# Performance work log

Measured on AMD Instinct MI355X. Metric: run time of the kernel, lower is better.

Reference implementation:

```python
import jax, jax.numpy as jnp
import numpy as np

N, D_IN, HID, NH = 16384, 2048, 2048, 16
HD = HID // NH  # head_size = 128


def setup_inputs() -> dict:
    key = jax.random.key(0)
    ks = jax.random.split(key, 8)
    s = 1.0 / np.sqrt(D_IN)
    return {
        "protein": jax.random.normal(ks[0], (N, D_IN), jnp.float32),
        "drug": jax.random.normal(ks[1], (N, D_IN), jnp.float32),
        "mask_prot": jnp.ones((N,), bool),
        "mask_drug": jnp.ones((N,), bool),
        "Wq_p": jax.random.uniform(ks[2], (D_IN, HID), jnp.float32, -s, s),
        "Wk_p": jax.random.uniform(ks[3], (D_IN, HID), jnp.float32, -s, s),
        "Wv_p": jax.random.uniform(ks[4], (D_IN, HID), jnp.float32, -s, s),
        "Wq_d": jax.random.uniform(ks[5], (D_IN, HID), jnp.float32, -s, s),
        "Wk_d": jax.random.uniform(ks[6], (D_IN, HID), jnp.float32, -s, s),
        "Wv_d": jax.random.uniform(ks[7], (D_IN, HID), jnp.float32, -s, s),
    }


def _heads(x):
    # [N, L, HID] -> [N, L, NH, HD]
    return x.reshape(x.shape[0], x.shape[1], NH, HD)


def _alpha_logits(logits, mask_row, mask_col, inf=1e6):
    # logits: [N, L1, L2, H]; masks: [N, L1], [N, L2] (broadcast over heads)
    mask_pair = mask_row[:, :, None, None] & mask_col[:, None, :, None]
    logits = jnp.where(mask_pair, logits, logits - inf)
    alpha = jax.nn.softmax(logits, axis=2)
    alpha = jnp.where(mask_row[:, :, None, None], alpha, jnp.zeros_like(alpha))
    return alpha


def reference(protein, drug, mask_prot, mask_drug, Wq_p, Wk_p, Wv_p, Wq_d, Wk_d, Wv_d):
    p = protein[:, None, :]  # [N, 1, D_IN]
    d = drug[:, None, :]
    # forward() overwrites the masks with all-ones of shape [N, L=1]
    m_p = jnp.ones(p.shape[:-1], bool)
    m_d = jnp.ones(d.shape[:-1], bool)

    qp = _heads(jnp.einsum('bld,dh->blh', p, Wq_p))  # [N,1,NH,HD]
    kp = _heads(jnp.einsum('bld,dh->blh', p, Wk_p))
    vp = _heads(jnp.einsum('bld,dh->blh', p, Wv_p))
    qd = _heads(jnp.einsum('bld,dh->blh', d, Wq_d))
    kd = _heads(jnp.einsum('bld,dh->blh', d, Wk_d))
    vd = _heads(jnp.einsum('bld,dh->blh', d, Wv_d))

    logits_pp = jnp.einsum('blhd,bkhd->blkh', qp, kp)
    logits_pd = jnp.einsum('blhd,bkhd->blkh', qp, kd)
    logits_dp = jnp.einsum('blhd,bkhd->blkh', qd, kp)
    logits_dd = jnp.einsum('blhd,bkhd->blkh', qd, kd)

    a_pp = _alpha_logits(logits_pp, m_p, m_p)
    a_pd = _alpha_logits(logits_pd, m_p, m_d)
    a_dp = _alpha_logits(logits_dp, m_d, m_p)
    a_dd = _alpha_logits(logits_dd, m_d, m_d)

    def agg(alpha, v):
        out = jnp.einsum('blkh,bkhd->blhd', alpha, v)
        return out.reshape(out.shape[0], out.shape[1], HID)

    prot_embedding = (agg(a_pp, vp) + agg(a_pd, vd)) / 2  # [N,1,HID]
    drug_embedding = (agg(a_dp, vp) + agg(a_dd, vd)) / 2

    # agg_mode == 'cls'
    prot_embed = prot_embedding[:, 0]
    drug_embed = drug_embedding[:, 0]
    return jnp.concatenate([prot_embed, drug_embed], axis=1)  # [N, 2*HID]
```

## Files before the change

### kernel.cpp

```cpp
#include <hip/hip_runtime.h>
#include <stdint.h>


typedef __attribute__((ext_vector_type(8))) short short8;
typedef __attribute__((ext_vector_type(4))) float float4v;
typedef __attribute__((ext_vector_type(2))) unsigned int uint2v;

typedef const __attribute__((address_space(1))) unsigned int* gp_t;
typedef __attribute__((address_space(3))) unsigned int* lp_t;

#define M_DIM 16384
#define N_DIM 2048
#define K_DIM 4096
#define OUT_LD 4096

static __device__ __forceinline__ unsigned int pack_bf16x2(float x, float y) {
  union { float f; unsigned int u; } a, b;
  a.f = x; b.f = y;
  unsigned int ua = a.u + 0x8000u;
  unsigned int ub = b.u + 0x8000u;
  return __builtin_amdgcn_perm(ub, ua, 0x07060302u);
}

static __device__ __forceinline__ unsigned short f2bf(float x) {
  union { float f; unsigned int u; } a; a.f = x;
  return (unsigned short)((a.u + 0x8000u) >> 16);
}

__global__ __launch_bounds__(256)
void prep_wt(const float* __restrict__ Wp, const float* __restrict__ Wd,
             unsigned short* __restrict__ Wt) {
  __shared__ float tile[32][33];
  const int k0 = blockIdx.x * 32;
  const int n0 = blockIdx.y * 32;
  const int tx = threadIdx.x;
  const int ty = threadIdx.y;
  const float* W = (k0 < 2048) ? Wp : Wd;
  const int kk0 = (k0 < 2048) ? k0 : k0 - 2048;
#pragma unroll
  for (int i = 0; i < 4; ++i) {
    int r = ty * 4 + i;
    tile[r][tx] = W[(size_t)(kk0 + r) * 2048 + n0 + tx];
  }
  __syncthreads();
#pragma unroll
  for (int i = 0; i < 4; ++i) {
    int r = ty * 4 + i;
    Wt[(size_t)(n0 + r) * (size_t)K_DIM + k0 + tx] = f2bf(tile[tx][r]);
  }
}

__global__ __launch_bounds__(256)
void cast_a(const float* __restrict__ P, const float* __restrict__ Dg,
            unsigned int* __restrict__ Abf) {
  int idx = blockIdx.x * 256 + threadIdx.x;
  int row = idx >> 10;
  int j = (idx & 1023) << 2;
  const float* src = (j < 2048) ? (P + (size_t)row * 2048 + j)
                                : (Dg + (size_t)row * 2048 + (j - 2048));
  float4v v = *(const float4v*)src;
  uint2v o;
  o.x = pack_bf16x2(v.x, v.y);
  o.y = pack_bf16x2(v.z, v.w);
  *(uint2v*)(Abf + (size_t)row * 2048 + (j >> 1)) = o;
}


#define VMW(N) asm volatile("s_waitcnt vmcnt(" #N ")" ::: "memory")
#define LGW0() asm volatile("s_waitcnt lgkmcnt(0)" ::: "memory")
#define BAR() __builtin_amdgcn_s_barrier()
#define SP1 __builtin_amdgcn_s_setprio(1);
#define SP0 __builtin_amdgcn_s_setprio(0);

__global__ __launch_bounds__(512, 1)
void gemm8(const unsigned short* __restrict__ Abf,
           const unsigned short* __restrict__ Wt,
           float* __restrict__ out) {
  __shared__ unsigned short As[2][256 * 64];
  __shared__ unsigned short Bs[2][256 * 64];

  const int t = threadIdx.x;
  const int w = t >> 6, l = t & 63;
  const int wm = w >> 2, wn = w & 3;
  const int lr = l & 15, q16 = l >> 4, xr = lr & 7;

  const int bx = blockIdx.x;
  const int logical = (bx & 7) * 64 + (bx >> 3);
  const int tn = logical & 7, tm = logical >> 3;
  const int m0 = tm << 8, n0 = tn << 8;

  const int srow = t >> 3;
  const int sk = (((t & 7) ^ (srow & 7)) << 3);
  const int brr = srow & 31;
  const int bsel = t >> 8;

  auto stage_a = [&](int buf, int k0, int h) {
#pragma unroll
    for (int sub = 0; sub < 2; ++sub) {
      const int row = m0 + sub * 128 + h * 64 + srow;
      const unsigned short* g = Abf + (size_t)row * K_DIM + (k0 + sk);
      const int ldsrow0 = sub * 128 + h * 64 + (w << 3);
      __builtin_amdgcn_global_load_lds((gp_t)(const void*)g,
                                       (lp_t)&As[buf][ldsrow0 * 64], 16, 0, 0);
    }
  };
  auto stage_b = [&](int buf, int k0, int nh) {
#pragma unroll
    for (int sub = 0; sub < 2; ++sub) {
      const int wnr = sub * 2 + bsel;
      const int ncol = n0 + wnr * 64 + nh * 32 + brr;
      const unsigned short* g = Wt + (size_t)ncol * K_DIM + (k0 + sk);
      const int ldsrow0 = wnr * 64 + nh * 32 + ((w & 3) << 3);
      __builtin_amdgcn_global_load_lds((gp_t)(const void*)g,
                                       (lp_t)&Bs[buf][ldsrow0 * 64], 16, 0, 0);
    }
  };

  float4v acc[8][4];
#pragma unroll
  for (int i = 0; i < 8; ++i)
#pragma unroll
    for (int j = 0; j < 4; ++j)
      acc[i][j] = (float4v){0.f, 0.f, 0.f, 0.f};

  const int aoff = (wm * 128 + lr) * 64;
  const int boff = (wn * 64 + lr) * 64;
  const int c0 = (q16 ^ xr) << 3;
  const int c1 = ((4 + q16) ^ xr) << 3;

  short8 aR[8][2];
  short8 bR[4][2];

  stage_a(0, 0, 0);
  stage_a(0, 0, 1);
  stage_b(0, 0, 0);
  stage_b(0, 0, 1);
  stage_a(1, 64, 0);
  stage_b(1, 64, 0);
  stage_b(1, 64, 1);
  stage_a(1, 64, 1);
  VMW(8);
  BAR();
  {
    const unsigned short* Ac = &As[0][0];
    const unsigned short* Bc = &Bs[0][0];
#pragma unroll
    for (int i = 0; i < 8; ++i) {
      aR[i][0] = *(const short8*)&Ac[aoff + i * 1024 + c0];
      aR[i][1] = *(const short8*)&Ac[aoff + i * 1024 + c1];
    }
#pragma unroll
    for (int j = 0; j < 4; ++j) {
      bR[j][0] = *(const short8*)&Bc[boff + j * 1024 + c0];
      bR[j][1] = *(const short8*)&Bc[boff + j * 1024 + c1];
    }
  }
  LGW0();
  BAR();

  auto tile_mfma = [&](const unsigned short* AcN, const unsigned short* BcN,
                       bool doread) {
    SP1
#pragma unroll
    for (int ks = 0; ks < 2; ++ks) {
      const int cks = ks ? c1 : c0;
#pragma unroll
      for (int i = 0; i < 8; ++i) {
#pragma unroll
        for (int j = 0; j < 4; ++j)
          acc[i][j] = __builtin_amdgcn_mfma_f32_16x16x32_bf16(
              aR[i][ks], bR[j][ks], acc[i][j], 0, 0, 0);
        if (doread)
          aR[i][ks] = *(const short8*)&AcN[aoff + i * 1024 + cks];
      }
      if (doread) {
#pragma unroll
        for (int j = 0; j < 4; ++j)
          bR[j][ks] = *(const short8*)&BcN[boff + j * 1024 + cks];
      }
    }
    SP0
  };

  for (int tt = 0; tt < 62; ++tt) {
    const int buf = tt & 1;
    const int k2 = tt * 64 + 128;
    stage_a(buf, k2, 0);
    stage_a(buf, k2, 1);
    stage_b(buf, k2, 0);
    stage_b(buf, k2, 1);
    tile_mfma(&As[buf ^ 1][0], &Bs[buf ^ 1][0], true);
    VMW(0);
    LGW0();
    BAR();
  }

  tile_mfma(&As[1][0], &Bs[1][0], true);
  tile_mfma(nullptr, nullptr, false);

  const int rbase = m0 + wm * 128 + q16 * 4;
  const int cbase = n0 + wn * 64 + lr;
#pragma unroll
  for (int f = 0; f < 8; ++f)
#pragma unroll
    for (int j = 0; j < 4; ++j) {
      const int row = rbase + f * 16;
      const int col = cbase + j * 16;
#pragma unroll
      for (int r = 0; r < 4; ++r) {
        float v = acc[f][j][r] * 0.5f;
        size_t o = (size_t)(row + r) * (size_t)OUT_LD + col;
        out[o] = v;
        out[o + N_DIM] = v;
      }
    }
}

__global__ __launch_bounds__(256)
void gemm_k(const float* __restrict__ Ap, const float* __restrict__ Ad,
            const unsigned short* __restrict__ Wt,
            float* __restrict__ out) {
  __shared__ unsigned short As[128 * 64];
  __shared__ unsigned short Bsm[128 * 64];

  const int t = threadIdx.x;
  const int bx = blockIdx.x;
  const int tn = bx & 15, tm = bx >> 4;
  const int m0 = tm << 7, n0 = tn << 7;
  const int w = t >> 6, l = t & 63;
  const int wmm = w & 1, wnn = w >> 1;
  const int lr = l & 15, q = l >> 4;

  const int rB = t >> 3;
  const int kB = (t & 7) * 8;

  float4v acc[4][4];
#pragma unroll
  for (int i = 0; i < 4; ++i)
#pragma unroll
    for (int j = 0; j < 4; ++j)
      acc[i][j] = (float4v){0.f, 0.f, 0.f, 0.f};

  for (int k0 = 0; k0 < K_DIM; k0 += 64) {
#pragma unroll
    for (int i = 0; i < 4; ++i) {
      const unsigned short* g =
          Wt + (size_t)(n0 + i * 32 + rB) * (size_t)K_DIM + (k0 + kB);
      __builtin_amdgcn_global_load_lds((gp_t)(const void*)g,
                                       (lp_t)&Bsm[i * 2048 + w * 512], 16, 0, 0);
    }
    {
      const float* base;
      int kk;
      if (k0 < 2048) { base = Ap; kk = k0; } else { base = Ad; kk = k0 - 2048; }
      const int rA = t >> 4;
      const int cA = (t & 15) * 4;
#pragma unroll
      for (int i = 0; i < 8; ++i) {
        int m = i * 16 + rA;
        float4v v = *(const float4v*)(base + (size_t)(m0 + m) * 2048 + kk + cA);
        uint2v o;
        o.x = pack_bf16x2(v.x, v.y);
        o.y = pack_bf16x2(v.z, v.w);
        *(uint2v*)&As[m * 64 + cA] = o;
      }
    }
    __syncthreads();

#pragma unroll
    for (int ks = 0; ks < 2; ++ks) {
      short8 a2[4], b2[4];
#pragma unroll
      for (int i = 0; i < 4; ++i) {
        a2[i] = *(const short8*)&As[(wmm * 64 + i * 16 + lr) * 64 + ks * 32 + q * 8];
        b2[i] = *(const short8*)&Bsm[(wnn * 64 + i * 16 + lr) * 64 + ks * 32 + q * 8];
      }
#pragma unroll
      for (int i = 0; i < 4; ++i)
#pragma unroll
        for (int j = 0; j < 4; ++j)
          acc[i][j] = __builtin_amdgcn_mfma_f32_16x16x32_bf16(a2[i], b2[j],
                                                              acc[i][j], 0, 0, 0);
    }
    __syncthreads();
  }

#pragma unroll
  for (int i = 0; i < 4; ++i) {
    const int r0 = m0 + wmm * 64 + i * 16 + q * 4;
#pragma unroll
    for (int j = 0; j < 4; ++j) {
      const int c = n0 + wnn * 64 + j * 16 + lr;
#pragma unroll
      for (int r = 0; r < 4; ++r) {
        float v = acc[i][j][r] * 0.5f;
        size_t o = (size_t)(r0 + r) * (size_t)OUT_LD + c;
        out[o] = v;
        out[o + 2048] = v;
      }
    }
  }
}

__global__ __launch_bounds__(256)
void gemm_fallback(const float* __restrict__ P, const float* __restrict__ Dg,
                   const float* __restrict__ Wp, const float* __restrict__ Wd,
                   float* __restrict__ out) {
  __shared__ float Asf[64][17];
  __shared__ float Bsf[16][65];
  const int bx = blockIdx.x;
  const int by = blockIdx.y;
  const int t = threadIdx.x;
  const int tc = t & 15, trw = t >> 4;
  const int m0 = by * 64, n0 = bx * 64;
  float accf[4][4] = {};
  for (int k0 = 0; k0 < 4096; k0 += 16) {
    const float* Asrc = (k0 < 2048) ? P : Dg;
    const float* Bsrc = (k0 < 2048) ? Wp : Wd;
    const int kk = k0 & 2047;
#pragma unroll
    for (int i = 0; i < 4; ++i) {
      int r = i * 16 + trw;
      Asf[r][tc] = Asrc[(size_t)(m0 + r) * 2048 + kk + tc];
    }
#pragma unroll
    for (int i = 0; i < 4; ++i) {
      int r = i * 4 + (t >> 6);
      int c = t & 63;
      Bsf[r][c] = Bsrc[(size_t)(kk + r) * 2048 + n0 + c];
    }
    __syncthreads();
#pragma unroll
    for (int k2 = 0; k2 < 16; ++k2) {
      float a[4], b[4];
#pragma unroll
      for (int i = 0; i < 4; ++i) a[i] = Asf[trw * 4 + i][k2];
#pragma unroll
      for (int j = 0; j < 4; ++j) b[j] = Bsf[k2][tc * 4 + j];
#pragma unroll
      for (int i = 0; i < 4; ++i)
#pragma unroll
        for (int j = 0; j < 4; ++j) accf[i][j] += a[i] * b[j];
    }
    __syncthreads();
  }
#pragma unroll
  for (int i = 0; i < 4; ++i)
#pragma unroll
    for (int j = 0; j < 4; ++j) {
      float v = accf[i][j] * 0.5f;
      size_t o = (size_t)(m0 + trw * 4 + i) * 4096 + n0 + tc * 4 + j;
      out[o] = v;
      out[o + 2048] = v;
    }
}

extern "C" void kernel_launch(void* const* d_in, const int* in_sizes, int n_in,
                              void* d_out, int out_size, void* d_ws, size_t ws_size,
                              hipStream_t stream) {
  const float* protein = (const float*)d_in[0];
  const float* drug    = (const float*)d_in[1];
  const float* Wv_p    = (const float*)d_in[6];
  const float* Wv_d    = (const float*)d_in[9];
  float* out = (float*)d_out;

  const size_t wt_bytes = (size_t)N_DIM * K_DIM * sizeof(unsigned short);
  const size_t a_bytes  = (size_t)M_DIM * K_DIM * sizeof(unsigned short);

  if (ws_size >= wt_bytes) {
    unsigned short* Wt = (unsigned short*)d_ws;
    prep_wt<<<dim3(128, 64), dim3(32, 8), 0, stream>>>(Wv_p, Wv_d, Wt);
    if (ws_size >= wt_bytes + a_bytes) {
      unsigned int* Abf = (unsigned int*)((char*)d_ws + wt_bytes);
      cast_a<<<65536, 256, 0, stream>>>(protein, drug, Abf);
      gemm8<<<512, 512, 0, stream>>>((const unsigned short*)Abf, Wt, out);
    } else {
      gemm_k<<<2048, 256, 0, stream>>>(protein, drug, Wt, out);
    }
  } else {
    gemm_fallback<<<dim3(32, 256), 256, 0, stream>>>(protein, drug, Wv_p, Wv_d, out);
  }
}
```

Measured before the change: 754.6 us.

## Load GEMM B operand directly from global into registers, bypassing LDS

The weight (B) tile is no longer staged through shared memory with async global-to-LDS copies. Each wave now reads its B fragments straight from global memory into registers, one k-tile ahead. The wait before the barrier is relaxed so that only the A staging loads must finish. This halves LDS footprint and LDS read traffic, but it duplicates B global reads across waves that share a column block. It also exposes global load latency with only one tile of MFMA work to hide it.

```diff
diff --git a/kernel.cpp b/kernel.cpp
--- a/kernel.cpp
+++ b/kernel.cpp
@@ -65,7 +65,6 @@
   *(uint2v*)(Abf + (size_t)row * 2048 + (j >> 1)) = o;
 }
 
-
 #define VMW(N) asm volatile("s_waitcnt vmcnt(" #N ")" ::: "memory")
 #define LGW0() asm volatile("s_waitcnt lgkmcnt(0)" ::: "memory")
 #define BAR() __builtin_amdgcn_s_barrier()
@@ -77,7 +76,6 @@
            const unsigned short* __restrict__ Wt,
            float* __restrict__ out) {
   __shared__ unsigned short As[2][256 * 64];
-  __shared__ unsigned short Bs[2][256 * 64];
 
   const int t = threadIdx.x;
   const int w = t >> 6, l = t & 63;
@@ -91,8 +89,6 @@
 
   const int srow = t >> 3;
   const int sk = (((t & 7) ^ (srow & 7)) << 3);
-  const int brr = srow & 31;
-  const int bsel = t >> 8;
 
   auto stage_a = [&](int buf, int k0, int h) {
 #pragma unroll
@@ -104,17 +100,6 @@
                                        (lp_t)&As[buf][ldsrow0 * 64], 16, 0, 0);
     }
   };
-  auto stage_b = [&](int buf, int k0, int nh) {
-#pragma unroll
-    for (int sub = 0; sub < 2; ++sub) {
-      const int wnr = sub * 2 + bsel;
-      const int ncol = n0 + wnr * 64 + nh * 32 + brr;
-      const unsigned short* g = Wt + (size_t)ncol * K_DIM + (k0 + sk);
-      const int ldsrow0 = wnr * 64 + nh * 32 + ((w & 3) << 3);
-      __builtin_amdgcn_global_load_lds((gp_t)(const void*)g,
-                                       (lp_t)&Bs[buf][ldsrow0 * 64], 16, 0, 0);
-    }
-  };
 
   float4v acc[8][4];
 #pragma unroll
@@ -124,42 +109,41 @@
       acc[i][j] = (float4v){0.f, 0.f, 0.f, 0.f};
 
   const int aoff = (wm * 128 + lr) * 64;
-  const int boff = (wn * 64 + lr) * 64;
   const int c0 = (q16 ^ xr) << 3;
   const int c1 = ((4 + q16) ^ xr) << 3;
 
+  const unsigned short* bBase[4];
+#pragma unroll
+  for (int j = 0; j < 4; ++j)
+    bBase[j] = Wt + (size_t)(n0 + wn * 64 + j * 16 + lr) * (size_t)K_DIM +
+               q16 * 8;
+
   short8 aR[8][2];
   short8 bR[4][2];
 
   stage_a(0, 0, 0);
   stage_a(0, 0, 1);
-  stage_b(0, 0, 0);
-  stage_b(0, 0, 1);
   stage_a(1, 64, 0);
-  stage_b(1, 64, 0);
-  stage_b(1, 64, 1);
   stage_a(1, 64, 1);
+#pragma unroll
+  for (int j = 0; j < 4; ++j) {
+    bR[j][0] = *(const short8*)&bBase[j][0];
+    bR[j][1] = *(const short8*)&bBase[j][32];
+  }
   VMW(8);
   BAR();
   {
     const unsigned short* Ac = &As[0][0];
-    const unsigned short* Bc = &Bs[0][0];
 #pragma unroll
     for (int i = 0; i < 8; ++i) {
       aR[i][0] = *(const short8*)&Ac[aoff + i * 1024 + c0];
       aR[i][1] = *(const short8*)&Ac[aoff + i * 1024 + c1];
     }
-#pragma unroll
-    for (int j = 0; j < 4; ++j) {
-      bR[j][0] = *(const short8*)&Bc[boff + j * 1024 + c0];
-      bR[j][1] = *(const short8*)&Bc[boff + j * 1024 + c1];
-    }
   }
   LGW0();
   BAR();
 
-  auto tile_mfma = [&](const unsigned short* AcN, const unsigned short* BcN,
-                       bool doread) {
+  auto tile_mfma = [&](const unsigned short* AcN, int kN, bool doread) {
     SP1
 #pragma unroll
     for (int ks = 0; ks < 2; ++ks) {
@@ -176,7 +160,7 @@
       if (doread) {
 #pragma unroll
         for (int j = 0; j < 4; ++j)
-          bR[j][ks] = *(const short8*)&BcN[boff + j * 1024 + cks];
+          bR[j][ks] = *(const short8*)&bBase[j][kN + ks * 32];
       }
     }
     SP0
@@ -185,18 +169,17 @@
   for (int tt = 0; tt < 62; ++tt) {
     const int buf = tt & 1;
     const int k2 = tt * 64 + 128;
+    const int k1 = tt * 64 + 64;
     stage_a(buf, k2, 0);
     stage_a(buf, k2, 1);
-    stage_b(buf, k2, 0);
-    stage_b(buf, k2, 1);
-    tile_mfma(&As[buf ^ 1][0], &Bs[buf ^ 1][0], true);
-    VMW(0);
+    tile_mfma(&As[buf ^ 1][0], k1, true);
+    VMW(8);
     LGW0();
     BAR();
   }
 
-  tile_mfma(&As[1][0], &Bs[1][0], true);
-  tile_mfma(nullptr, nullptr, false);
+  tile_mfma(&As[1][0], 4032, true);
+  tile_mfma(nullptr, 0, false);
 
   const int rbase = m0 + wm * 128 + q16 * 4;
   const int cbase = n0 + wn * 64 + lr;
```

Result: slower. 841.3 us (+11.5%).
